# Kernel tuning notes

Measured on AMD Instinct MI355X. Metric: run time of the kernel, lower is better.

Reference implementation:

```python
import jax, jax.numpy as jnp
import numpy as np

N_VOX = 200000
Z, Y, X = 41, 256, 256


def _build_rulebook(N, seed=0):
    """Build submanifold 3x3x3 rulebook: nbr[i,k] = voxel index of neighbor k of voxel i, or -1."""
    rng = np.random.default_rng(seed)
    keys = np.unique(rng.integers(0, Z * Y * X, size=int(N * 1.3)))
    assert keys.shape[0] >= N
    keys = keys[:N]  # sorted unique linearized coords
    z = keys // (Y * X)
    rem = keys % (Y * X)
    y = rem // X
    x = rem % X
    nbr = np.full((N, 27), -1, np.int32)
    k = 0
    for dz in (-1, 0, 1):
        for dy in (-1, 0, 1):
            for dx in (-1, 0, 1):
                nz, ny, nx = z + dz, y + dy, x + dx
                valid = (nz >= 0) & (nz < Z) & (ny >= 0) & (ny < Y) & (nx >= 0) & (nx < X)
                nkey = (nz * Y + ny) * X + nx
                pos = np.searchsorted(keys, nkey)
                pos_c = np.minimum(pos, N - 1)
                found = valid & (keys[pos_c] == nkey)
                nbr[:, k] = np.where(found, pos_c, -1)
                k += 1
    return nbr


def setup_inputs() -> dict:
    key = jax.random.key(0)
    ks = jax.random.split(key, 8)
    nbr = jnp.asarray(_build_rulebook(N_VOX))
    return {
        "voxel_features": jax.random.normal(ks[0], (N_VOX, 4), jnp.float32),
        "nbr_idx": nbr,
        "W0": jax.random.normal(ks[1], (27, 4, 16), jnp.float32) * 0.05,
        "s0": jnp.ones((16,), jnp.float32),
        "b0": jnp.zeros((16,), jnp.float32),
        "W1": jax.random.normal(ks[2], (27, 16, 16), jnp.float32) * 0.05,
        "s1": jnp.ones((16,), jnp.float32),
        "b1": jnp.zeros((16,), jnp.float32),
        "W2": jax.random.normal(ks[3], (27, 16, 16), jnp.float32) * 0.05,
        "s2": jnp.ones((16,), jnp.float32),
        "b2": jnp.zeros((16,), jnp.float32),
        "W_lin": jax.random.normal(ks[4], (16, 3), jnp.float32) * 0.05,
        "b_lin": jnp.zeros((3,), jnp.float32),
    }


def _subm_conv(feats, W, nbr, mask):
    # feats: [N, Cin], W: [27, Cin, Cout], nbr: [N, 27] (rulebook), mask: [N, 27, 1]
    g = jnp.take(feats, jnp.maximum(nbr, 0), axis=0) * mask  # [N, 27, Cin] gather (memory-bound)
    return jnp.einsum("nkc,kcd->nd", g, W)  # scatter-free dense contraction


def reference(voxel_features, nbr_idx, W0, s0, b0, W1, s1, b1, W2, s2, b2, W_lin, b_lin):
    mask = (nbr_idx >= 0)[..., None].astype(voxel_features.dtype)
    # conv_input: SubMConv3d(4,16,3) + BN(folded to scale/shift) + ReLU
    x = jax.nn.relu(_subm_conv(voxel_features, W0, nbr_idx, mask) * s0 + b0)
    # SparseBasicBlock(16,16, indice_key='subm1'): conv-bn-relu-conv-bn + residual + relu
    idn = x
    h = jax.nn.relu(_subm_conv(x, W1, nbr_idx, mask) * s1 + b1)
    h = _subm_conv(h, W2, nbr_idx, mask) * s2 + b2
    x = jax.nn.relu(h + idn)
    # mos_seg_layer: Linear(16, mos_class)
    return x @ W_lin + b_lin
```

## Files before the change

kernel.cpp:

```cpp
#include <hip/hip_runtime.h>
#include <cstdint>

#define NVOX 200000
#define T1 128
#define NT1 ((NVOX + T1 - 1) / T1)
#define VPB 64
#define NT2 ((NVOX + VPB - 1) / VPB)
#define WPITCH 132

typedef _Float16 h2 __attribute__((ext_vector_type(2)));

__device__ __forceinline__ uint32_t packh2(float a, float b) {
    h2 v; v.x = (_Float16)a; v.y = (_Float16)b;
    return __builtin_bit_cast(uint32_t, v);
}
__device__ __forceinline__ h2 toh2(uint32_t u) { return __builtin_bit_cast(h2, u); }

__global__ __launch_bounds__(256) void k0_pack(const float* __restrict__ W1,
                                               const float* __restrict__ W2,
                                               uint32_t* __restrict__ wp1,
                                               uint32_t* __restrict__ wp2) {
    int i = blockIdx.x * 256 + threadIdx.x;
    if (i >= 2 * 3456) return;
    int half = i >= 3456;
    int r = i - half * 3456;
    const float* W = half ? W2 : W1;
    uint32_t* wp = half ? wp2 : wp1;
    int k = r >> 7, j = r & 127, d = j >> 3, p = j & 7;
    float a = W[(k * 16 + 2 * p) * 16 + d];
    float b = W[(k * 16 + 2 * p + 1) * 16 + d];
    wp[r] = packh2(a, b);
}

__global__ __launch_bounds__(128) void k1_compact_conv0(
    const float* __restrict__ feats,
    const int* __restrict__ nbr,
    const float* __restrict__ W,
    const float* __restrict__ s, const float* __restrict__ b,
    int* __restrict__ ent,
    int* __restrict__ cnt,
    uint32_t* __restrict__ xh) {
    __shared__ int   lnbr[T1 * 27];
    __shared__ __align__(16) float Wl[27 * 68];
    int t = threadIdx.x;
    int base = blockIdx.x * T1;
    for (int i = t; i < 27 * 64; i += T1)
        Wl[(i >> 6) * 68 + (i & 63)] = W[i];
    int nv = NVOX - base; if (nv > T1) nv = T1;
    const int* gsrc = nbr + base * 27;
    for (int i = t; i < nv * 27; i += T1)
        lnbr[i] = gsrc[i];
    __syncthreads();

    int n = base + t;
    if (t >= nv) return;
    int* row = lnbr + t * 27;
    int c = 0;
    #pragma unroll
    for (int k = 0; k < 27; ++k) {
        int idx = row[k];
        if (idx >= 0) {
            int e = (idx << 5) | k;
            row[c] = e;
            ent[c * NVOX + n] = e;
            ++c;
        }
    }
    cnt[n] = c;

    float acc[16];
    #pragma unroll
    for (int d = 0; d < 16; ++d) acc[d] = 0.f;
    int e = row[0];
    float4 f = *(const float4*)(feats + (e >> 5) * 4);
    int j = 0;
    while (true) {
        bool more = (++j < c);
        int en = e; float4 fn = f;
        if (more) {
            en = row[j];
            fn = *(const float4*)(feats + (en >> 5) * 4);
        }
        {
            const float4* wrow = (const float4*)(Wl + (e & 31) * 68);
            float g[4] = {f.x, f.y, f.z, f.w};
            #pragma unroll
            for (int cc = 0; cc < 4; ++cc) {
                float gc = g[cc];
                float4 w0 = wrow[cc * 4 + 0];
                float4 w1 = wrow[cc * 4 + 1];
                float4 w2 = wrow[cc * 4 + 2];
                float4 w3 = wrow[cc * 4 + 3];
                acc[0]  += gc * w0.x; acc[1]  += gc * w0.y; acc[2]  += gc * w0.z; acc[3]  += gc * w0.w;
                acc[4]  += gc * w1.x; acc[5]  += gc * w1.y; acc[6]  += gc * w1.z; acc[7]  += gc * w1.w;
                acc[8]  += gc * w2.x; acc[9]  += gc * w2.y; acc[10] += gc * w2.z; acc[11] += gc * w2.w;
                acc[12] += gc * w3.x; acc[13] += gc * w3.y; acc[14] += gc * w3.z; acc[15] += gc * w3.w;
            }
        }
        if (!more) break;
        e = en; f = fn;
    }
    float v[16];
    #pragma unroll
    for (int d = 0; d < 16; ++d) {
        float u = acc[d] * s[d] + b[d];
        v[d] = u > 0.f ? u : 0.f;
    }
    uint4 u0, u1;
    u0.x = packh2(v[0], v[1]);  u0.y = packh2(v[2], v[3]);
    u0.z = packh2(v[4], v[5]);  u0.w = packh2(v[6], v[7]);
    u1.x = packh2(v[8], v[9]);  u1.y = packh2(v[10], v[11]);
    u1.z = packh2(v[12], v[13]); u1.w = packh2(v[14], v[15]);
    ((uint4*)xh)[n * 2 + 0] = u0;
    ((uint4*)xh)[n * 2 + 1] = u1;
}

__device__ __forceinline__ void conv16_dot2(const uint32_t* __restrict__ fin,
                                            const int* __restrict__ ent,
                                            int c, int n, int d0,
                                            const uint32_t* __restrict__ wl,
                                            float acc[4]) {
    #pragma unroll
    for (int d = 0; d < 4; ++d) acc[d] = 0.f;
    if (c <= 0) return;
    int e = ent[n];
    const uint4* fp = (const uint4*)(fin + (e >> 5) * 8);
    uint4 fa = fp[0], fb = fp[1];
    int j = 0;
    while (true) {
        bool more = (++j < c);
        int en = e;
        uint4 ga = fa, gb = fb;
        if (more) {
            en = ent[j * NVOX + n];
            const uint4* fq = (const uint4*)(fin + (en >> 5) * 8);
            ga = fq[0]; gb = fq[1];
        }
        {
            int k = e & 31;
            h2 f0 = toh2(fa.x), f1 = toh2(fa.y), f2 = toh2(fa.z), f3 = toh2(fa.w);
            h2 f4 = toh2(fb.x), f5 = toh2(fb.y), f6 = toh2(fb.z), f7 = toh2(fb.w);
            const uint32_t* wk = wl + k * WPITCH + d0 * 8;
            #pragma unroll
            for (int dd = 0; dd < 4; ++dd) {
                uint4 wa = *(const uint4*)(wk + dd * 8);
                uint4 wb = *(const uint4*)(wk + dd * 8 + 4);
                float a = acc[dd];
                a = __builtin_amdgcn_fdot2(f0, toh2(wa.x), a, false);
                a = __builtin_amdgcn_fdot2(f1, toh2(wa.y), a, false);
                a = __builtin_amdgcn_fdot2(f2, toh2(wa.z), a, false);
                a = __builtin_amdgcn_fdot2(f3, toh2(wa.w), a, false);
                a = __builtin_amdgcn_fdot2(f4, toh2(wb.x), a, false);
                a = __builtin_amdgcn_fdot2(f5, toh2(wb.y), a, false);
                a = __builtin_amdgcn_fdot2(f6, toh2(wb.z), a, false);
                a = __builtin_amdgcn_fdot2(f7, toh2(wb.w), a, false);
                acc[dd] = a;
            }
        }
        if (!more) break;
        e = en; fa = ga; fb = gb;
    }
}

__device__ __forceinline__ void stage_and_rank(const uint32_t* __restrict__ wp,
                                               const int* __restrict__ cnt,
                                               uint32_t* __restrict__ wl,
                                               int* __restrict__ lcnt, int* __restrict__ lperm,
                                               int base, int t) {
    for (int i = t; i < 3456; i += 256)
        wl[(i >> 7) * WPITCH + (i & 127)] = wp[i];
    if (t < VPB) {
        int n = base + t;
        lcnt[t] = (n < NVOX) ? cnt[n] : 0;
    }
    __syncthreads();
    if (t < VPB) {
        int me = lcnt[t];
        int r = 0;
        #pragma unroll 8
        for (int j2 = 0; j2 < VPB; ++j2) {
            int oj = lcnt[j2];
            r += (oj < me) || (oj == me && j2 < t);
        }
        lperm[r] = t;
    }
    __syncthreads();
}

__global__ __launch_bounds__(256, 6) void k2_conv1(
    const uint32_t* __restrict__ xh,
    const int* __restrict__ ent, const int* __restrict__ cnt,
    const uint32_t* __restrict__ wp,
    const float* __restrict__ s, const float* __restrict__ b,
    uint32_t* __restrict__ hh) {
    __shared__ __align__(16) uint32_t wl[27 * WPITCH];
    __shared__ int lcnt[VPB];
    __shared__ int lperm[VPB];
    int t = threadIdx.x;
    int base = blockIdx.x * VPB;
    stage_and_rank(wp, cnt, wl, lcnt, lperm, base, t);
    int g = t >> 2, cg = t & 3;
    int lv = lperm[g];
    int n = base + lv;
    bool valid = n < NVOX;
    int c = lcnt[lv];
    int d0 = cg * 4;
    float acc[4];
    conv16_dot2(xh, ent, valid ? c : 0, n, d0, wl, acc);
    if (!valid) return;
    float v[4];
    #pragma unroll
    for (int dd = 0; dd < 4; ++dd) {
        float u = acc[dd] * s[d0 + dd] + b[d0 + dd];
        v[dd] = u > 0.f ? u : 0.f;
    }
    uint2 o;
    o.x = packh2(v[0], v[1]);
    o.y = packh2(v[2], v[3]);
    *(uint2*)(hh + n * 8 + cg * 2) = o;
}

__global__ __launch_bounds__(256, 6) void k3_conv2_final(
    const uint32_t* __restrict__ hh,
    const int* __restrict__ ent, const int* __restrict__ cnt,
    const uint32_t* __restrict__ wp,
    const float* __restrict__ s, const float* __restrict__ b,
    const uint32_t* __restrict__ xh,
    const float* __restrict__ Wlin,
    const float* __restrict__ blin,
    float* __restrict__ out) {
    __shared__ __align__(16) uint32_t wl[27 * WPITCH];
    __shared__ int lcnt[VPB];
    __shared__ int lperm[VPB];
    int t = threadIdx.x;
    int base = blockIdx.x * VPB;
    stage_and_rank(wp, cnt, wl, lcnt, lperm, base, t);
    int g = t >> 2, cg = t & 3;
    int lv = lperm[g];
    int n = base + lv;
    bool valid = n < NVOX;
    int c = lcnt[lv];
    int d0 = cg * 4;
    float acc[4];
    conv16_dot2(hh, ent, valid ? c : 0, n, d0, wl, acc);
    float o0 = 0.f, o1 = 0.f, o2 = 0.f;
    if (valid) {
        uint2 iv = *(const uint2*)(xh + n * 8 + cg * 2);
        h2 i0 = toh2(iv.x), i1 = toh2(iv.y);
        float idn[4] = {(float)i0.x, (float)i0.y, (float)i1.x, (float)i1.y};
        #pragma unroll
        for (int dd = 0; dd < 4; ++dd) {
            int d = d0 + dd;
            float u = acc[dd] * s[d] + b[d] + idn[dd];
            u = u > 0.f ? u : 0.f;
            o0 += u * Wlin[d * 3 + 0];
            o1 += u * Wlin[d * 3 + 1];
            o2 += u * Wlin[d * 3 + 2];
        }
    }
    o0 += __shfl_xor(o0, 1); o0 += __shfl_xor(o0, 2);
    o1 += __shfl_xor(o1, 1); o1 += __shfl_xor(o1, 2);
    o2 += __shfl_xor(o2, 1); o2 += __shfl_xor(o2, 2);
    if (valid && cg == 0) {
        out[n * 3 + 0] = o0 + blin[0];
        out[n * 3 + 1] = o1 + blin[1];
        out[n * 3 + 2] = o2 + blin[2];
    }
}

extern "C" void kernel_launch(void* const* d_in, const int* in_sizes, int n_in,
                              void* d_out, int out_size, void* d_ws, size_t ws_size,
                              hipStream_t stream) {
    const float* feats = (const float*)d_in[0];
    const int*   nbr   = (const int*)d_in[1];
    const float* W0    = (const float*)d_in[2];
    const float* s0    = (const float*)d_in[3];
    const float* b0    = (const float*)d_in[4];
    const float* W1    = (const float*)d_in[5];
    const float* s1    = (const float*)d_in[6];
    const float* b1    = (const float*)d_in[7];
    const float* W2    = (const float*)d_in[8];
    const float* s2    = (const float*)d_in[9];
    const float* b2    = (const float*)d_in[10];
    const float* Wlin  = (const float*)d_in[11];
    const float* blin  = (const float*)d_in[12];
    float* out = (float*)d_out;

    char* ws = (char*)d_ws;
    int*      ent = (int*)(ws);
    int*      cnt = (int*)(ws + 21600000);
    uint32_t* xh  = (uint32_t*)(ws + 22400000);
    uint32_t* hh  = (uint32_t*)(ws + 28800000);
    uint32_t* wp1 = (uint32_t*)(ws + 35200000);
    uint32_t* wp2 = (uint32_t*)(ws + 35213824);

    k0_pack<<<27, 256, 0, stream>>>(W1, W2, wp1, wp2);
    k1_compact_conv0<<<NT1, T1, 0, stream>>>(feats, nbr, W0, s0, b0, ent, cnt, xh);
    k2_conv1<<<NT2, 256, 0, stream>>>(xh, ent, cnt, wp1, s1, b1, hh);
    k3_conv2_final<<<NT2, 256, 0, stream>>>(hh, ent, cnt, wp2, s2, b2, xh, Wlin, blin, out);
}
```

Before: 76.94 us.

## Batch four gathers per iteration and sort conv0 voxels by neighbor count

Result: no change. 76.01 us (-1.2%).

```diff
diff --git a/kernel.cpp b/kernel.cpp
--- a/kernel.cpp
+++ b/kernel.cpp
@@ -32,6 +32,24 @@
     wp[r] = packh2(a, b);
 }
 
+__device__ __forceinline__ void conv0_entry(int e, float4 f, const float* __restrict__ Wl,
+                                            float acc[16]) {
+    const float4* wrow = (const float4*)(Wl + (e & 31) * 68);
+    float g[4] = {f.x, f.y, f.z, f.w};
+    #pragma unroll
+    for (int cc = 0; cc < 4; ++cc) {
+        float gc = g[cc];
+        float4 w0 = wrow[cc * 4 + 0];
+        float4 w1 = wrow[cc * 4 + 1];
+        float4 w2 = wrow[cc * 4 + 2];
+        float4 w3 = wrow[cc * 4 + 3];
+        acc[0]  += gc * w0.x; acc[1]  += gc * w0.y; acc[2]  += gc * w0.z; acc[3]  += gc * w0.w;
+        acc[4]  += gc * w1.x; acc[5]  += gc * w1.y; acc[6]  += gc * w1.z; acc[7]  += gc * w1.w;
+        acc[8]  += gc * w2.x; acc[9]  += gc * w2.y; acc[10] += gc * w2.z; acc[11] += gc * w2.w;
+        acc[12] += gc * w3.x; acc[13] += gc * w3.y; acc[14] += gc * w3.z; acc[15] += gc * w3.w;
+    }
+}
+
 __global__ __launch_bounds__(128) void k1_compact_conv0(
     const float* __restrict__ feats,
     const int* __restrict__ nbr,
@@ -42,6 +60,8 @@
     uint32_t* __restrict__ xh) {
     __shared__ int   lnbr[T1 * 27];
     __shared__ __align__(16) float Wl[27 * 68];
+    __shared__ int   lcnt[T1];
+    __shared__ int   lperm[T1];
     int t = threadIdx.x;
     int base = blockIdx.x * T1;
     for (int i = t; i < 27 * 64; i += T1)
@@ -52,53 +72,60 @@
         lnbr[i] = gsrc[i];
     __syncthreads();
 
-    int n = base + t;
-    if (t >= nv) return;
-    int* row = lnbr + t * 27;
     int c = 0;
-    #pragma unroll
-    for (int k = 0; k < 27; ++k) {
-        int idx = row[k];
-        if (idx >= 0) {
-            int e = (idx << 5) | k;
-            row[c] = e;
-            ent[c * NVOX + n] = e;
-            ++c;
+    {
+        int* row = lnbr + t * 27;
+        if (t < nv) {
+            #pragma unroll
+            for (int k = 0; k < 27; ++k) {
+                int idx = row[k];
+                if (idx >= 0) {
+                    int e = (idx << 5) | k;
+                    row[c] = e;
+                    ent[c * NVOX + (base + t)] = e;
+                    ++c;
+                }
+            }
+            cnt[base + t] = c;
         }
     }
-    cnt[n] = c;
+    lcnt[t] = c;
+    __syncthreads();
+    {
+        int me = lcnt[t];
+        int r = 0;
+        for (int j2 = 0; j2 < T1; ++j2) {
+            int oj = lcnt[j2];
+            r += (oj < me) || (oj == me && j2 < t);
+        }
+        lperm[r] = t;
+    }
+    __syncthreads();
+
+    int lv = lperm[t];
+    int cc2 = lcnt[lv];
+    if (cc2 == 0) return;
+    const int* row = lnbr + lv * 27;
+    int n = base + lv;
 
     float acc[16];
     #pragma unroll
     for (int d = 0; d < 16; ++d) acc[d] = 0.f;
-    int e = row[0];
-    float4 f = *(const float4*)(feats + (e >> 5) * 4);
     int j = 0;
-    while (true) {
-        bool more = (++j < c);
-        int en = e; float4 fn = f;
-        if (more) {
-            en = row[j];
-            fn = *(const float4*)(feats + (en >> 5) * 4);
-        }
-        {
-            const float4* wrow = (const float4*)(Wl + (e & 31) * 68);
-            float g[4] = {f.x, f.y, f.z, f.w};
-            #pragma unroll
-            for (int cc = 0; cc < 4; ++cc) {
-                float gc = g[cc];
-                float4 w0 = wrow[cc * 4 + 0];
-                float4 w1 = wrow[cc * 4 + 1];
-                float4 w2 = wrow[cc * 4 + 2];
-                float4 w3 = wrow[cc * 4 + 3];
-                acc[0]  += gc * w0.x; acc[1]  += gc * w0.y; acc[2]  += gc * w0.z; acc[3]  += gc * w0.w;
-                acc[4]  += gc * w1.x; acc[5]  += gc * w1.y; acc[6]  += gc * w1.z; acc[7]  += gc * w1.w;
-                acc[8]  += gc * w2.x; acc[9]  += gc * w2.y; acc[10] += gc * w2.z; acc[11] += gc * w2.w;
-                acc[12] += gc * w3.x; acc[13] += gc * w3.y; acc[14] += gc * w3.z; acc[15] += gc * w3.w;
-            }
-        }
-        if (!more) break;
-        e = en; f = fn;
+    while (j < cc2) {
+        int m = cc2 - j; if (m > 4) m = 4;
+        int e0 = 0, e1 = 0, e2 = 0, e3 = 0;
+        float4 f0, f1, f2, f3;
+        e0 = row[j];
+        f0 = *(const float4*)(feats + (e0 >> 5) * 4);
+        if (m > 1) { e1 = row[j + 1]; f1 = *(const float4*)(feats + (e1 >> 5) * 4); }
+        if (m > 2) { e2 = row[j + 2]; f2 = *(const float4*)(feats + (e2 >> 5) * 4); }
+        if (m > 3) { e3 = row[j + 3]; f3 = *(const float4*)(feats + (e3 >> 5) * 4); }
+        conv0_entry(e0, f0, Wl, acc);
+        if (m > 1) conv0_entry(e1, f1, Wl, acc);
+        if (m > 2) conv0_entry(e2, f2, Wl, acc);
+        if (m > 3) conv0_entry(e3, f3, Wl, acc);
+        j += m;
     }
     float v[16];
     #pragma unroll
@@ -107,12 +134,35 @@
         v[d] = u > 0.f ? u : 0.f;
     }
     uint4 u0, u1;
-    u0.x = packh2(v[0], v[1]);  u0.y = packh2(v[2], v[3]);
-    u0.z = packh2(v[4], v[5]);  u0.w = packh2(v[6], v[7]);
-    u1.x = packh2(v[8], v[9]);  u1.y = packh2(v[10], v[11]);
+    u0.x = packh2(v[0], v[1]);   u0.y = packh2(v[2], v[3]);
+    u0.z = packh2(v[4], v[5]);   u0.w = packh2(v[6], v[7]);
+    u1.x = packh2(v[8], v[9]);   u1.y = packh2(v[10], v[11]);
     u1.z = packh2(v[12], v[13]); u1.w = packh2(v[14], v[15]);
     ((uint4*)xh)[n * 2 + 0] = u0;
     ((uint4*)xh)[n * 2 + 1] = u1;
+}
+
+__device__ __forceinline__ void dot2_entry(int e, uint4 fa, uint4 fb, int d0,
+                                           const uint32_t* __restrict__ wl, float acc[4]) {
+    int k = e & 31;
+    h2 f0 = toh2(fa.x), f1 = toh2(fa.y), f2 = toh2(fa.z), f3 = toh2(fa.w);
+    h2 f4 = toh2(fb.x), f5 = toh2(fb.y), f6 = toh2(fb.z), f7 = toh2(fb.w);
+    const uint32_t* wk = wl + k * WPITCH + d0 * 8;
+    #pragma unroll
+    for (int dd = 0; dd < 4; ++dd) {
+        uint4 wa = *(const uint4*)(wk + dd * 8);
+        uint4 wb = *(const uint4*)(wk + dd * 8 + 4);
+        float a = acc[dd];
+        a = __builtin_amdgcn_fdot2(f0, toh2(wa.x), a, false);
+        a = __builtin_amdgcn_fdot2(f1, toh2(wa.y), a, false);
+        a = __builtin_amdgcn_fdot2(f2, toh2(wa.z), a, false);
+        a = __builtin_amdgcn_fdot2(f3, toh2(wa.w), a, false);
+        a = __builtin_amdgcn_fdot2(f4, toh2(wb.x), a, false);
+        a = __builtin_amdgcn_fdot2(f5, toh2(wb.y), a, false);
+        a = __builtin_amdgcn_fdot2(f6, toh2(wb.z), a, false);
+        a = __builtin_amdgcn_fdot2(f7, toh2(wb.w), a, false);
+        acc[dd] = a;
+    }
 }
 
 __device__ __forceinline__ void conv16_dot2(const uint32_t* __restrict__ fin,
@@ -123,42 +173,24 @@
     #pragma unroll
     for (int d = 0; d < 4; ++d) acc[d] = 0.f;
     if (c <= 0) return;
-    int e = ent[n];
-    const uint4* fp = (const uint4*)(fin + (e >> 5) * 8);
-    uint4 fa = fp[0], fb = fp[1];
     int j = 0;
-    while (true) {
-        bool more = (++j < c);
-        int en = e;
-        uint4 ga = fa, gb = fb;
-        if (more) {
-            en = ent[j * NVOX + n];
-            const uint4* fq = (const uint4*)(fin + (en >> 5) * 8);
-            ga = fq[0]; gb = fq[1];
-        }
-        {
-            int k = e & 31;
-            h2 f0 = toh2(fa.x), f1 = toh2(fa.y), f2 = toh2(fa.z), f3 = toh2(fa.w);
-            h2 f4 = toh2(fb.x), f5 = toh2(fb.y), f6 = toh2(fb.z), f7 = toh2(fb.w);
-            const uint32_t* wk = wl + k * WPITCH + d0 * 8;
-            #pragma unroll
-            for (int dd = 0; dd < 4; ++dd) {
-                uint4 wa = *(const uint4*)(wk + dd * 8);
-                uint4 wb = *(const uint4*)(wk + dd * 8 + 4);
-                float a = acc[dd];
-                a = __builtin_amdgcn_fdot2(f0, toh2(wa.x), a, false);
-                a = __builtin_amdgcn_fdot2(f1, toh2(wa.y), a, false);
-                a = __builtin_amdgcn_fdot2(f2, toh2(wa.z), a, false);
-                a = __builtin_amdgcn_fdot2(f3, toh2(wa.w), a, false);
-                a = __builtin_amdgcn_fdot2(f4, toh2(wb.x), a, false);
-                a = __builtin_amdgcn_fdot2(f5, toh2(wb.y), a, false);
-                a = __builtin_amdgcn_fdot2(f6, toh2(wb.z), a, false);
-                a = __builtin_amdgcn_fdot2(f7, toh2(wb.w), a, false);
-                acc[dd] = a;
-            }
-        }
-        if (!more) break;
-        e = en; fa = ga; fb = gb;
+    while (j < c) {
+        int m = c - j; if (m > 4) m = 4;
+        int e0 = 0, e1 = 0, e2 = 0, e3 = 0;
+        uint4 fa0, fb0, fa1, fb1, fa2, fb2, fa3, fb3;
+        e0 = ent[j * NVOX + n];
+        if (m > 1) e1 = ent[(j + 1) * NVOX + n];
+        if (m > 2) e2 = ent[(j + 2) * NVOX + n];
+        if (m > 3) e3 = ent[(j + 3) * NVOX + n];
+        { const uint4* fq = (const uint4*)(fin + (e0 >> 5) * 8); fa0 = fq[0]; fb0 = fq[1]; }
+        if (m > 1) { const uint4* fq = (const uint4*)(fin + (e1 >> 5) * 8); fa1 = fq[0]; fb1 = fq[1]; }
+        if (m > 2) { const uint4* fq = (const uint4*)(fin + (e2 >> 5) * 8); fa2 = fq[0]; fb2 = fq[1]; }
+        if (m > 3) { const uint4* fq = (const uint4*)(fin + (e3 >> 5) * 8); fa3 = fq[0]; fb3 = fq[1]; }
+        dot2_entry(e0, fa0, fb0, d0, wl, acc);
+        if (m > 1) dot2_entry(e1, fa1, fb1, d0, wl, acc);
+        if (m > 2) dot2_entry(e2, fa2, fb2, d0, wl, acc);
+        if (m > 3) dot2_entry(e3, fa3, fb3, d0, wl, acc);
+        j += m;
     }
 }
 
```
